# Kernel tuning notes

Measured on AMD Instinct MI355X. Metric: run time of the kernel, lower is better.

## Reference

```python
import jax, jax.numpy as jnp
import numpy as np

N = 100000       # nodes
E0 = 1600000     # edges without self loops
E = E0 + N       # with self loops appended (attr 0), matching add_self_loops
DIN = 128        # input_dim
HID = 64         # nb_hidden_gnn (per-head out_channels)
HEADS = 4
EMB = 128
L = 3            # nb_layer
NEG_SLOPE = 0.2
BN_EPS = 1e-5


def setup_inputs() -> dict:
    key = jax.random.key(0)
    ks = jax.random.split(key, 12)
    # edges with no self loops; self loops (i,i) appended with edge_attr 0
    row = jax.random.randint(ks[0], (E0,), 0, N)
    off = jax.random.randint(ks[1], (E0,), 1, N)
    col = (row + off) % N
    loops = jnp.arange(N, dtype=row.dtype)
    edge_index = jnp.stack([jnp.concatenate([row, loops]),
                            jnp.concatenate([col, loops])])
    edge_attr = jnp.concatenate([jax.random.normal(ks[2], (E0, 1), jnp.float32),
                                 jnp.zeros((N, 1), jnp.float32)])
    x = jax.random.normal(ks[3], (N, DIN), jnp.float32)
    HC = HEADS * HID
    linN0 = jax.random.normal(ks[4], (DIN, HC)) * HC ** -0.5
    linN_rest = jax.random.normal(ks[5], (L - 1, HID, HC)) * HC ** -0.5
    linE_all = jax.random.normal(ks[6], (L, 1, HEADS)) * HEADS ** -0.5  # nb_edge_attr=1
    att_all = jax.random.normal(ks[7], (L, HEADS, 2 * HID + 1)) * (2 * HID + 1) ** -0.5
    bias_all = jnp.zeros((L, HID))  # concat=False -> bias [out_channels]
    bn_gamma = jnp.ones((L - 1, HID))
    bn_beta = jnp.zeros((L - 1, HID))
    W = jax.random.normal(ks[8], (HID, EMB)) * HID ** -0.5
    b = jnp.zeros((EMB,))
    return {"x": x, "edge_index": edge_index, "edge_attr": edge_attr,
            "linN0": linN0, "linN_rest": linN_rest, "linE_all": linE_all,
            "att_all": att_all, "bias_all": bias_all,
            "bn_gamma": bn_gamma, "bn_beta": bn_beta, "W": W, "b": b}


def _gcn_layer(x, row, col, edge_attr, linN, linE, att, bias, bn):
    n = x.shape[0]
    if bn is not None:
        gamma, beta = bn
        mu = x.mean(axis=0)
        var = x.var(axis=0)
        x = (x - mu) * jax.lax.rsqrt(var + BN_EPS) * gamma + beta
    h = (x @ linN).reshape(n, HEADS, HID)                 # [N,H,C]
    e = (edge_attr @ linE)                                # [E,H] (nb_edge_attr=1)
    att_i = att[:, :HID]                                  # [H,C]
    att_j = att[:, HID:2 * HID]                           # [H,C]
    att_e = att[:, 2 * HID:]                              # [H,1]
    # per-node partial scores avoid gathering full features twice
    s_i = jnp.einsum('nhc,hc->nh', h, att_i)
    s_j = jnp.einsum('nhc,hc->nh', h, att_j)
    logits = s_i[row] + s_j[col] + e * att_e[:, 0]        # [E,H]
    logits = jax.nn.leaky_relu(logits, NEG_SLOPE)
    # segment softmax over destination nodes (edge_index[1])
    m = jax.ops.segment_max(logits, col, num_segments=n)
    p = jnp.exp(logits - m[col])
    denom = jax.ops.segment_sum(p, col, num_segments=n)
    alpha = p / (denom[col] + 1e-16)
    # message: alpha * x[source], scatter-add to destination
    msg = alpha[:, :, None] * h[row]                      # [E,H,C]
    out = jax.ops.segment_sum(msg, col, num_segments=n)   # [N,H,C]
    out = out.mean(axis=1) + bias + h.mean(axis=1)        # concat=False, res=True
    return jax.nn.relu(out)


def reference(x, edge_index, edge_attr, linN0, linN_rest, linE_all, att_all,
              bias_all, bn_gamma, bn_beta, W, b):
    row, col = edge_index[0], edge_index[1]
    emb = x
    for l in range(L):
        linN = linN0 if l == 0 else linN_rest[l - 1]
        bn = None if l == 0 else (bn_gamma[l - 1], bn_beta[l - 1])
        emb = _gcn_layer(emb, row, col, edge_attr, linN, linE_all[l],
                         att_all[l], bias_all[l], bn)
    return emb @ W + b
```

## Files before the change

kernel.cpp:

```cpp
#include <hip/hip_runtime.h>
#include <math.h>

#define NN 100000
#define E0E 1600000
#define EE (E0E + NN)
#define NEG 0.2f
#define BNEPS 1e-5f
#define LOG2E 1.4426950408889634f

typedef float f4 __attribute__((ext_vector_type(4)));
typedef float f2 __attribute__((ext_vector_type(2)));
typedef short s8v __attribute__((ext_vector_type(8)));

__device__ __forceinline__ float wred_max(float v) {
#pragma unroll
  for (int m = 1; m < 64; m <<= 1) v = fmaxf(v, __shfl_xor(v, m, 64));
  return v;
}
__device__ __forceinline__ float wred_sum(float v) {
#pragma unroll
  for (int m = 1; m < 64; m <<= 1) v += __shfl_xor(v, m, 64);
  return v;
}
__device__ __forceinline__ float sel4(float a0, float a1, float a2, float a3, int hd) {
  return (hd & 2) ? ((hd & 1) ? a3 : a2) : ((hd & 1) ? a1 : a0);
}
__device__ __forceinline__ unsigned short f2bf(float x) {
  unsigned u = __float_as_uint(x);
  return (unsigned short)((u + 0x7fffu + ((u >> 16) & 1u)) >> 16);
}
__device__ __forceinline__ float bf2f(unsigned short s) {
  return __uint_as_float(((unsigned)s) << 16);
}
__device__ __forceinline__ void gll16(const void* g, void* l) {
  __builtin_amdgcn_global_load_lds(
      (const __attribute__((address_space(1))) void*)g,
      (__attribute__((address_space(3))) void*)l, 16, 0, 0);
}

__global__ void k_count(const int* __restrict__ col, int* cnt, int e) {
  int i = blockIdx.x * blockDim.x + threadIdx.x;
  if (i < e) atomicAdd(&cnt[col[i]], 1);
}
#define SCAN_T 1024
__global__ void k_scan1(const int* __restrict__ cnt, int* partial, int n, int chunk) {
  int i = blockIdx.x * blockDim.x + threadIdx.x;
  int beg = i * chunk, end = min(n, beg + chunk);
  int s = 0;
  for (int j = beg; j < end; ++j) s += cnt[j];
  partial[i] = s;
}
__global__ void k_scan2(int* partial) {
  __shared__ int lds[SCAN_T];
  int t = threadIdx.x;
  int v = partial[t];
  lds[t] = v;
  __syncthreads();
  for (int off = 1; off < SCAN_T; off <<= 1) {
    int add = (t >= off) ? lds[t - off] : 0;
    __syncthreads();
    lds[t] += add;
    __syncthreads();
  }
  partial[t] = lds[t] - v;
}
__global__ void k_scan3(const int* __restrict__ cnt, const int* __restrict__ partial,
                        int* rowptr, int* cursor, int n, int chunk, int etot) {
  int i = blockIdx.x * blockDim.x + threadIdx.x;
  int beg = i * chunk, end = min(n, beg + chunk);
  int run = partial[i];
  for (int j = beg; j < end; ++j) {
    rowptr[j] = run;
    cursor[j] = run;
    run += cnt[j];
  }
  if (i == SCAN_T - 1) rowptr[n] = etot;
}
__global__ void k_scatter(const int* __restrict__ row, const int* __restrict__ col,
                          const float* __restrict__ ea, int* cursor, int2* csr, int e) {
  int i = blockIdx.x * blockDim.x + threadIdx.x;
  if (i < e) {
    int c = col[i];
    int p = atomicAdd(&cursor[c], 1);
    csr[p] = make_int2(row[i], __float_as_int(ea[i]));
  }
}

__global__ void k_bnstats(const unsigned short* __restrict__ x, double* sums, int n) {
  int f = threadIdx.x & 63;
  int rt = (blockIdx.x * blockDim.x + threadIdx.x) >> 6;
  int rstride = (gridDim.x * blockDim.x) >> 6;
  double s = 0.0, q = 0.0;
  for (int r = rt; r < n; r += rstride) {
    double v = (double)bf2f(x[(size_t)r * 64 + f]);
    s += v;
    q += v * v;
  }
  __shared__ double ls[256], lq[256];
  ls[threadIdx.x] = s;
  lq[threadIdx.x] = q;
  __syncthreads();
  if (threadIdx.x < 64) {
    s = ls[threadIdx.x] + ls[threadIdx.x + 64] + ls[threadIdx.x + 128] + ls[threadIdx.x + 192];
    q = lq[threadIdx.x] + lq[threadIdx.x + 64] + lq[threadIdx.x + 128] + lq[threadIdx.x + 192];
    atomicAdd(&sums[f], s);
    atomicAdd(&sums[64 + f], q);
  }
}

__global__ void k_prepw(const float* __restrict__ W, const double* __restrict__ bnsum,
                        const float* __restrict__ gamma, const float* __restrict__ beta,
                        const float* __restrict__ bin, unsigned short* __restrict__ Wt,
                        float* __restrict__ cvec, int K, int N, int mode) {
  __shared__ float ABl[128];
  __shared__ float cred[4][64];
  int t = threadIdx.x;
  if (mode == 1) {
    if (t < 64) {
      double mean = bnsum[t] / NN;
      double var = bnsum[64 + t] / NN - mean * mean;
      float A = gamma[t] * rsqrtf((float)var + BNEPS);
      ABl[t] = A;
      ABl[64 + t] = beta[t] - (float)mean * A;
    }
    __syncthreads();
  }
  int cl = t & 63, kq = t >> 6;
  int col = blockIdx.x * 64 + cl;
  int kn = K >> 2;
  int k0 = kq * kn;
  float c = 0.f;
#pragma unroll 8
  for (int k = k0; k < k0 + kn; ++k) {
    float w = W[k * N + col];
    float a = 1.f, b = 0.f;
    if (mode == 1) { a = ABl[k]; b = ABl[64 + k]; }
    Wt[col * K + k] = f2bf(a * w);
    c = fmaf(b, w, c);
  }
  cred[kq][cl] = c;
  __syncthreads();
  if (kq == 0) {
    float cc = cred[0][cl] + cred[1][cl] + cred[2][cl] + cred[3][cl];
    if (mode == 2) cc += bin[col];
    cvec[col] = cc;
  }
}

template <int K, int CT, bool ATT, bool OB, bool INBF>
__global__ __launch_bounds__(256, 2) void k_gemm(const void* __restrict__ xv,
                                                 const unsigned short* __restrict__ Wt,
                                                 const float* __restrict__ cvec,
                                                 const float* __restrict__ att,
                                                 void* __restrict__ houtv,
                                                 float* __restrict__ s_i,
                                                 float* __restrict__ s_j, int n,
                                                 int ntiles) {
  constexpr int KS = K / 32;
  constexpr int ROWB = 2 * K;
  constexpr int CPR = K / 8;
  constexpr int NCOL = 4 * CT * 16;
  __shared__ unsigned char xs[64 * ROWB];
  const int lane = threadIdx.x & 63;
  const int wv = threadIdx.x >> 6;
  const int l15 = lane & 15;
  const int lq = lane >> 4;
  const int colbase = wv * CT * 16;

  s8v wfr[CT][KS];
#pragma unroll
  for (int ct = 0; ct < CT; ++ct)
#pragma unroll
    for (int ks = 0; ks < KS; ++ks)
      wfr[ct][ks] = *(const s8v*)&Wt[(size_t)(colbase + ct * 16 + l15) * K + ks * 32 + lq * 8];
  float cb[CT][4];
#pragma unroll
  for (int ct = 0; ct < CT; ++ct)
#pragma unroll
    for (int r = 0; r < 4; ++r) cb[ct][r] = cvec[colbase + ct * 16 + lq * 4 + r];
  float ati[ATT ? CT : 1][4], atj[ATT ? CT : 1][4];
  if constexpr (ATT) {
    const float* ar = att + wv * 129;
#pragma unroll
    for (int ct = 0; ct < CT; ++ct)
#pragma unroll
      for (int r = 0; r < 4; ++r) {
        int cc = ct * 16 + lq * 4 + r;
        ati[ct][r] = ar[cc];
        atj[ct][r] = ar[64 + cc];
      }
  }

  for (int t = blockIdx.x; t < ntiles; t += gridDim.x) {
    const int row0 = t * 64;
    __syncthreads();
    if constexpr (INBF) {
      const unsigned char* xin8 = (const unsigned char*)xv;
#pragma unroll
      for (int i = 0; i < (64 * CPR) / 256; ++i) {
        int cbase = i * 256 + wv * 64;
        int c = cbase + lane;
        int row = c / CPR, kc = c % CPR;
        int rg = min(row0 + row, n - 1);
        int swz = kc ^ (row & 7);
        gll16(xin8 + (size_t)rg * ROWB + swz * 16, &xs[cbase * 16]);
      }
    } else {
#pragma unroll
      for (int i = 0; i < (64 * CPR) / 256; ++i) {
        int c = threadIdx.x + i * 256;
        int row = c / CPR, kc = c % CPR;
        int rg = min(row0 + row, n - 1);
        int dst = row * ROWB + ((kc * 16) ^ ((row & 7) << 4));
        const float* xin = (const float*)xv;
        const float* xp = xin + (size_t)rg * K + kc * 8;
        f4 a0 = *(const f4*)xp;
        f4 a1 = *(const f4*)(xp + 4);
        union { s8v v; unsigned short u[8]; } pk;
        pk.u[0] = f2bf(a0[0]); pk.u[1] = f2bf(a0[1]); pk.u[2] = f2bf(a0[2]); pk.u[3] = f2bf(a0[3]);
        pk.u[4] = f2bf(a1[0]); pk.u[5] = f2bf(a1[1]); pk.u[6] = f2bf(a1[2]); pk.u[7] = f2bf(a1[3]);
        *(s8v*)&xs[dst] = pk.v;
      }
    }
    __syncthreads();
    f4 acc[4][CT];
#pragma unroll
    for (int rt = 0; rt < 4; ++rt)
#pragma unroll
      for (int ct = 0; ct < CT; ++ct) acc[rt][ct] = (f4)0.f;
#pragma unroll
    for (int ks = 0; ks < KS; ++ks) {
      s8v xf[4];
#pragma unroll
      for (int rt = 0; rt < 4; ++rt) {
        int row = rt * 16 + l15;
        int kb = ks * 64 + lq * 16;
        xf[rt] = *(const s8v*)&xs[row * ROWB + (kb ^ ((row & 7) << 4))];
      }
#pragma unroll
      for (int rt = 0; rt < 4; ++rt)
#pragma unroll
        for (int ct = 0; ct < CT; ++ct)
          acc[rt][ct] = __builtin_amdgcn_mfma_f32_16x16x32_bf16(wfr[ct][ks], xf[rt],
                                                                acc[rt][ct], 0, 0, 0);
    }
#pragma unroll
    for (int rt = 0; rt < 4; ++rt) {
      if (row0 + rt * 16 >= n) continue;
      const size_t xrow = (size_t)(row0 + rt * 16 + l15);
      float v[CT][4];
#pragma unroll
      for (int ct = 0; ct < CT; ++ct)
#pragma unroll
        for (int r = 0; r < 4; ++r) v[ct][r] = acc[rt][ct][r] + cb[ct][r];
      if constexpr (OB) {
        float* outp = (float*)houtv;
#pragma unroll
        for (int ct = 0; ct < CT; ++ct) {
          f4 o;
          o[0] = v[ct][0]; o[1] = v[ct][1]; o[2] = v[ct][2]; o[3] = v[ct][3];
          *(f4*)&outp[xrow * NCOL + colbase + ct * 16 + lq * 4] = o;
        }
      } else {
        unsigned short* hout = (unsigned short*)houtv;
#pragma unroll
        for (int ct = 0; ct < CT; ++ct) {
          ushort4 hb4;
          hb4.x = f2bf(v[ct][0]); hb4.y = f2bf(v[ct][1]);
          hb4.z = f2bf(v[ct][2]); hb4.w = f2bf(v[ct][3]);
          *(ushort4*)&hout[xrow * NCOL + colbase + ct * 16 + lq * 4] = hb4;
        }
      }
      if constexpr (ATT) {
        float pi = 0.f, pj = 0.f;
#pragma unroll
        for (int ct = 0; ct < CT; ++ct)
#pragma unroll
          for (int r = 0; r < 4; ++r) {
            pi = fmaf(v[ct][r], ati[ct][r], pi);
            pj = fmaf(v[ct][r], atj[ct][r], pj);
          }
        pi += __shfl_xor(pi, 16, 64); pi += __shfl_xor(pi, 32, 64);
        pj += __shfl_xor(pj, 16, 64); pj += __shfl_xor(pj, 32, 64);
        if (lane < 16) {
          s_i[xrow * 4 + wv] = pi;
          s_j[xrow * 4 + wv] = pj;
        }
      }
    }
  }
}

__global__ __launch_bounds__(256) void k_edge(const int* __restrict__ rowptr,
                                              const int2* __restrict__ csr,
                                              const float* __restrict__ s_i,
                                              const float* __restrict__ s_j,
                                              const unsigned short* __restrict__ hb,
                                              const float* __restrict__ linE,
                                              const float* __restrict__ att,
                                              const float* __restrict__ bias,
                                              unsigned short* __restrict__ xout, int n) {
  __shared__ float lp[4][64][4];
  __shared__ int lsrc[4][64];
  const unsigned char* hb8 = (const unsigned char*)hb;
  const int lane = threadIdx.x & 63;
  const int wid = threadIdx.x >> 6;
  const int lane8 = lane * 8;
  int v = blockIdx.x * 4 + wid;
  if (v >= n) return;
  v = __builtin_amdgcn_readfirstlane(v);
  const int base = rowptr[v];
  const int deg = rowptr[v + 1] - base;

  const float coef0 = linE[0] * att[0 * 129 + 128];
  const float coef1 = linE[1] * att[1 * 129 + 128];
  const float coef2 = linE[2] * att[2 * 129 + 128];
  const float coef3 = linE[3] * att[3 * 129 + 128];
  const float sj0 = s_j[(size_t)v * 4 + 0];
  const float sj1 = s_j[(size_t)v * 4 + 1];
  const float sj2 = s_j[(size_t)v * 4 + 2];
  const float sj3 = s_j[(size_t)v * 4 + 3];

  auto edge_logits = [&](int i, int& src, float& g0, float& g1, float& g2, float& g3) {
    int2 pk = csr[i];
    src = pk.x;
    float ea = __int_as_float(pk.y);
    f4 siv = *(const f4*)&s_i[(size_t)src * 4];
    g0 = siv[0] + sj0 + ea * coef0; g0 = fmaxf(g0, g0 * NEG);
    g1 = siv[1] + sj1 + ea * coef1; g1 = fmaxf(g1, g1 * NEG);
    g2 = siv[2] + sj2 + ea * coef2; g2 = fmaxf(g2, g2 * NEG);
    g3 = siv[3] + sj3 + ea * coef3; g3 = fmaxf(g3, g3 * NEG);
  };

  const int hd = lane >> 4;
  f4 acc;
  {
    ushort4 hr = *(const ushort4*)(hb8 + ((unsigned)v << 9) + lane8);
    acc[0] = bf2f(hr.x); acc[1] = bf2f(hr.y); acc[2] = bf2f(hr.z); acc[3] = bf2f(hr.w);
  }

  bool fast = (deg <= 64);
  if (fast) {
    float g0 = -INFINITY, g1 = -INFINITY, g2 = -INFINITY, g3 = -INFINITY;
    int src = 0;
    bool valid = lane < deg;
    if (valid) edge_logits(base + lane, src, g0, g1, g2, g3);
    float m0 = wred_max(g0), m1 = wred_max(g1), m2 = wred_max(g2), m3 = wred_max(g3);
    float p0 = valid ? exp2f((g0 - m0) * LOG2E) : 0.f;
    float p1 = valid ? exp2f((g1 - m1) * LOG2E) : 0.f;
    float p2 = valid ? exp2f((g2 - m2) * LOG2E) : 0.f;
    float p3 = valid ? exp2f((g3 - m3) * LOG2E) : 0.f;
    float d0 = wred_sum(p0), d1 = wred_sum(p1), d2 = wred_sum(p2), d3 = wred_sum(p3);
    float rd0 = 1.f / (d0 + 1e-16f);
    float rd1 = 1.f / (d1 + 1e-16f);
    float rd2 = 1.f / (d2 + 1e-16f);
    float rd3 = 1.f / (d3 + 1e-16f);
    if (valid) {
      f4 pp;
      pp[0] = p0 * rd0; pp[1] = p1 * rd1; pp[2] = p2 * rd2; pp[3] = p3 * rd3;
      *(f4*)&lp[wid][lane][0] = pp;
      lsrc[wid][lane] = src << 9;
    }
    for (int e = 0; e < deg; ++e) {
      int off = lsrc[wid][e];
      float a = lp[wid][e][hd];
      ushort4 h0 = *(const ushort4*)(hb8 + (unsigned)(off + lane8));
      acc[0] = fmaf(a, bf2f(h0.x), acc[0]);
      acc[1] = fmaf(a, bf2f(h0.y), acc[1]);
      acc[2] = fmaf(a, bf2f(h0.z), acc[2]);
      acc[3] = fmaf(a, bf2f(h0.w), acc[3]);
    }
  } else {
    float m0 = -INFINITY, m1 = -INFINITY, m2 = -INFINITY, m3 = -INFINITY;
    for (int c0 = 0; c0 < deg; c0 += 64) {
      int i = c0 + lane;
      if (i < deg) {
        int src; float g0, g1, g2, g3;
        edge_logits(base + i, src, g0, g1, g2, g3);
        m0 = fmaxf(m0, g0); m1 = fmaxf(m1, g1); m2 = fmaxf(m2, g2); m3 = fmaxf(m3, g3);
      }
    }
    m0 = wred_max(m0); m1 = wred_max(m1); m2 = wred_max(m2); m3 = wred_max(m3);
    float d0 = 0, d1 = 0, d2 = 0, d3 = 0;
    for (int c0 = 0; c0 < deg; c0 += 64) {
      int i = c0 + lane;
      if (i < deg) {
        int src; float g0, g1, g2, g3;
        edge_logits(base + i, src, g0, g1, g2, g3);
        d0 += exp2f((g0 - m0) * LOG2E);
        d1 += exp2f((g1 - m1) * LOG2E);
        d2 += exp2f((g2 - m2) * LOG2E);
        d3 += exp2f((g3 - m3) * LOG2E);
      }
    }
    d0 = wred_sum(d0); d1 = wred_sum(d1); d2 = wred_sum(d2); d3 = wred_sum(d3);
    float msel = sel4(m0, m1, m2, m3, hd);
    float rdsel = 1.f / (sel4(d0, d1, d2, d3, hd) + 1e-16f);
    const float sjsel = sel4(sj0, sj1, sj2, sj3, hd);
    const float cfsel = sel4(coef0, coef1, coef2, coef3, hd);
    for (int e = base; e < base + deg; ++e) {
      int2 pk = csr[e];
      int src = pk.x;
      float ea = __int_as_float(pk.y);
      f4 siv = *(const f4*)&s_i[(size_t)src * 4];
      float lg = sel4(siv[0], siv[1], siv[2], siv[3], hd) + sjsel + ea * cfsel;
      lg = fmaxf(lg, lg * NEG);
      float a = exp2f((lg - msel) * LOG2E) * rdsel;
      ushort4 hr = *(const ushort4*)(hb8 + ((unsigned)src << 9) + lane8);
      acc[0] = fmaf(a, bf2f(hr.x), acc[0]);
      acc[1] = fmaf(a, bf2f(hr.y), acc[1]);
      acc[2] = fmaf(a, bf2f(hr.z), acc[2]);
      acc[3] = fmaf(a, bf2f(hr.w), acc[3]);
    }
  }
#pragma unroll
  for (int m = 16; m < 64; m <<= 1) {
    acc[0] += __shfl_xor(acc[0], m, 64);
    acc[1] += __shfl_xor(acc[1], m, 64);
    acc[2] += __shfl_xor(acc[2], m, 64);
    acc[3] += __shfl_xor(acc[3], m, 64);
  }
  if (lane < 16) {
    f4 bv = *(const f4*)&bias[lane * 4];
    ushort4 o;
    o.x = f2bf(fmaxf(acc[0] * 0.25f + bv[0], 0.f));
    o.y = f2bf(fmaxf(acc[1] * 0.25f + bv[1], 0.f));
    o.z = f2bf(fmaxf(acc[2] * 0.25f + bv[2], 0.f));
    o.w = f2bf(fmaxf(acc[3] * 0.25f + bv[3], 0.f));
    *(ushort4*)&xout[(size_t)v * 64 + lane * 4] = o;
  }
}

extern "C" void kernel_launch(void* const* d_in, const int* in_sizes, int n_in,
                              void* d_out, int out_size, void* d_ws, size_t ws_size,
                              hipStream_t stream) {
  const float* x_in = (const float*)d_in[0];
  const int* ei = (const int*)d_in[1];
  const float* eattr = (const float*)d_in[2];
  const float* linN0 = (const float*)d_in[3];
  const float* linNr = (const float*)d_in[4];
  const float* linE = (const float*)d_in[5];
  const float* attA = (const float*)d_in[6];
  const float* biasA = (const float*)d_in[7];
  const float* bng = (const float*)d_in[8];
  const float* bnb = (const float*)d_in[9];
  const float* W = (const float*)d_in[10];
  const float* bb = (const float*)d_in[11];
  float* out = (float*)d_out;

  const int* row = ei;
  const int* col = ei + EE;

  char* ws = (char*)d_ws;
  size_t o = 0;
  auto alloc = [&](size_t bytes) {
    void* p = ws + o;
    o += (bytes + 255) & ~(size_t)255;
    return p;
  };
  int* cnt = (int*)alloc((size_t)NN * 4);
  int* cursor = (int*)alloc((size_t)NN * 4);
  int* rowptr = (int*)alloc((size_t)(NN + 1) * 4);
  int* partial = (int*)alloc((size_t)SCAN_T * 4);
  int2* csr = (int2*)alloc((size_t)EE * 8);
  unsigned short* h = (unsigned short*)alloc((size_t)NN * 256 * 2);
  float* si = (float*)alloc((size_t)NN * 4 * 4);
  float* sj = (float*)alloc((size_t)NN * 4 * 4);
  unsigned short* xa = (unsigned short*)alloc((size_t)NN * 64 * 2);
  unsigned short* xb = (unsigned short*)alloc((size_t)NN * 64 * 2);
  double* bnsum = (double*)alloc(256 * 8);
  unsigned short* Wt = (unsigned short*)alloc((size_t)256 * 128 * 2);
  unsigned short* Wt2 = (unsigned short*)alloc((size_t)128 * 64 * 2);
  float* cvec = (float*)alloc(256 * 4);
  float* cvec2 = (float*)alloc(256 * 4);
  if (o > ws_size) return;

  const int chunk = (NN + SCAN_T - 1) / SCAN_T;
  const int NTILES = (NN + 63) / 64;
  const int GG = 512;

  hipMemsetAsync(cnt, 0, (size_t)NN * 4, stream);
  hipMemsetAsync(bnsum, 0, 256 * 8, stream);
  k_count<<<(EE + 255) / 256, 256, 0, stream>>>(col, cnt, EE);
  k_scan1<<<4, 256, 0, stream>>>(cnt, partial, NN, chunk);
  k_scan2<<<1, SCAN_T, 0, stream>>>(partial);
  k_scan3<<<4, 256, 0, stream>>>(cnt, partial, rowptr, cursor, NN, chunk, EE);
  k_scatter<<<(EE + 255) / 256, 256, 0, stream>>>(row, col, eattr, cursor, csr, EE);
  k_prepw<<<2, 256, 0, stream>>>(W, nullptr, nullptr, nullptr, bb, Wt2, cvec2, 64, 128, 2);

  k_prepw<<<4, 256, 0, stream>>>(linN0, nullptr, nullptr, nullptr, nullptr, Wt, cvec, 128, 256, 0);
  k_gemm<128, 4, true, false, false><<<GG, 256, 0, stream>>>(x_in, Wt, cvec, attA + 0,
                                                             h, si, sj, NN, NTILES);
  k_edge<<<NN / 4, 256, 0, stream>>>(rowptr, csr, si, sj, h, linE + 0, attA + 0, biasA + 0,
                                     xa, NN);

  k_bnstats<<<256, 256, 0, stream>>>(xa, bnsum, NN);
  k_prepw<<<4, 256, 0, stream>>>(linNr, bnsum, bng, bnb, nullptr, Wt, cvec, 64, 256, 1);
  k_gemm<64, 4, true, false, true><<<GG, 256, 0, stream>>>(xa, Wt, cvec, attA + 516,
                                                           h, si, sj, NN, NTILES);
  k_edge<<<NN / 4, 256, 0, stream>>>(rowptr, csr, si, sj, h, linE + 4, attA + 516, biasA + 64,
                                     xb, NN);

  k_bnstats<<<256, 256, 0, stream>>>(xb, bnsum + 128, NN);
  k_prepw<<<4, 256, 0, stream>>>(linNr + 64 * 256, bnsum + 128, bng + 64, bnb + 64, nullptr,
                                 Wt, cvec, 64, 256, 1);
  k_gemm<64, 4, true, false, true><<<GG, 256, 0, stream>>>(xb, Wt, cvec, attA + 2 * 516,
                                                           h, si, sj, NN, NTILES);
  k_edge<<<NN / 4, 256, 0, stream>>>(rowptr, csr, si, sj, h, linE + 8, attA + 2 * 516,
                                     biasA + 128, xa, NN);

  k_gemm<64, 2, false, true, true><<<GG, 256, 0, stream>>>(xa, Wt2, cvec2, nullptr, out,
                                                           nullptr, nullptr, NN, NTILES);
}
```

Measured before the change: 839.2 us.

## Fuse BN stats with weight prep and double-buffer bf16 GEMM tile loads

Merges the BatchNorm statistics kernel with the following weight-folding kernel by having the last block (found through an atomic done counter and threadfence) compute the scale and shift and write the folded bf16 weights. It also merges the two initial weight-prep launches into one kernel. In the bf16-input GEMM it double-buffers the LDS tile, so the async global-to-LDS load of the next tile is issued before computing the current one. This removes several small kernel launches and hides load latency, at the cost of twice the LDS for those GEMMs and a single-block tail for the weight fold.

Measured after the change: 828.9 us. About the same (-1.2%).

```diff
diff --git a/kernel.cpp b/kernel.cpp
--- a/kernel.cpp
+++ b/kernel.cpp
@@ -9,7 +9,6 @@
 #define LOG2E 1.4426950408889634f
 
 typedef float f4 __attribute__((ext_vector_type(4)));
-typedef float f2 __attribute__((ext_vector_type(2)));
 typedef short s8v __attribute__((ext_vector_type(8)));
 
 __device__ __forceinline__ float wred_max(float v) {
@@ -86,7 +85,32 @@
   }
 }
 
-__global__ void k_bnstats(const unsigned short* __restrict__ x, double* sums, int n) {
+__global__ void k_prep0(const float* __restrict__ W1, unsigned short* __restrict__ Wt1,
+                        float* __restrict__ cvec1, const float* __restrict__ W2,
+                        const float* __restrict__ bin2, unsigned short* __restrict__ Wt2,
+                        float* __restrict__ cvec2) {
+  int b = blockIdx.x;
+  int t = threadIdx.x;
+  int cl = t & 63, kq = t >> 6;
+  if (b < 4) {
+    int col = b * 64 + cl;
+#pragma unroll 8
+    for (int k = kq * 32; k < kq * 32 + 32; ++k)
+      Wt1[col * 128 + k] = f2bf(W1[k * 256 + col]);
+    if (kq == 0) cvec1[col] = 0.f;
+  } else {
+    int col = (b - 4) * 64 + cl;
+#pragma unroll 8
+    for (int k = kq * 16; k < kq * 16 + 16; ++k)
+      Wt2[col * 64 + k] = f2bf(W2[k * 128 + col]);
+    if (kq == 0) cvec2[col] = bin2[col];
+  }
+}
+
+__global__ void k_bnprep(const unsigned short* __restrict__ x, double* sums, int* done,
+                         const float* __restrict__ gamma, const float* __restrict__ beta,
+                         const float* __restrict__ W, unsigned short* __restrict__ Wt,
+                         float* __restrict__ cvec, int n) {
   int f = threadIdx.x & 63;
   int rt = (blockIdx.x * blockDim.x + threadIdx.x) >> 6;
   int rstride = (gridDim.x * blockDim.x) >> 6;
@@ -105,46 +129,36 @@
     q = lq[threadIdx.x] + lq[threadIdx.x + 64] + lq[threadIdx.x + 128] + lq[threadIdx.x + 192];
     atomicAdd(&sums[f], s);
     atomicAdd(&sums[64 + f], q);
-  }
-}
-
-__global__ void k_prepw(const float* __restrict__ W, const double* __restrict__ bnsum,
-                        const float* __restrict__ gamma, const float* __restrict__ beta,
-                        const float* __restrict__ bin, unsigned short* __restrict__ Wt,
-                        float* __restrict__ cvec, int K, int N, int mode) {
+    __threadfence();
+  }
+  __syncthreads();
+  __shared__ int lastFlag;
+  if (threadIdx.x == 0) {
+    int old = atomicAdd(done, 1);
+    lastFlag = (old == (int)gridDim.x - 1);
+  }
+  __syncthreads();
+  if (!lastFlag) return;
   __shared__ float ABl[128];
-  __shared__ float cred[4][64];
-  int t = threadIdx.x;
-  if (mode == 1) {
-    if (t < 64) {
-      double mean = bnsum[t] / NN;
-      double var = bnsum[64 + t] / NN - mean * mean;
-      float A = gamma[t] * rsqrtf((float)var + BNEPS);
-      ABl[t] = A;
-      ABl[64 + t] = beta[t] - (float)mean * A;
-    }
-    __syncthreads();
-  }
-  int cl = t & 63, kq = t >> 6;
-  int col = blockIdx.x * 64 + cl;
-  int kn = K >> 2;
-  int k0 = kq * kn;
+  if (threadIdx.x < 64) {
+    int t = threadIdx.x;
+    double mean = atomicAdd(&sums[t], 0.0) / n;
+    double qq = atomicAdd(&sums[64 + t], 0.0);
+    double var = qq / n - mean * mean;
+    float A = gamma[t] * rsqrtf((float)var + BNEPS);
+    ABl[t] = A;
+    ABl[64 + t] = beta[t] - (float)mean * A;
+  }
+  __syncthreads();
+  int col = threadIdx.x;
   float c = 0.f;
 #pragma unroll 8
-  for (int k = k0; k < k0 + kn; ++k) {
-    float w = W[k * N + col];
-    float a = 1.f, b = 0.f;
-    if (mode == 1) { a = ABl[k]; b = ABl[64 + k]; }
-    Wt[col * K + k] = f2bf(a * w);
-    c = fmaf(b, w, c);
-  }
-  cred[kq][cl] = c;
-  __syncthreads();
-  if (kq == 0) {
-    float cc = cred[0][cl] + cred[1][cl] + cred[2][cl] + cred[3][cl];
-    if (mode == 2) cc += bin[col];
-    cvec[col] = cc;
-  }
+  for (int k = 0; k < 64; ++k) {
+    float w = W[k * 256 + col];
+    Wt[col * 64 + k] = f2bf(ABl[k] * w);
+    c = fmaf(ABl[64 + k], w, c);
+  }
+  cvec[col] = c;
 }
 
 template <int K, int CT, bool ATT, bool OB, bool INBF>
@@ -160,7 +174,8 @@
   constexpr int ROWB = 2 * K;
   constexpr int CPR = K / 8;
   constexpr int NCOL = 4 * CT * 16;
-  __shared__ unsigned char xs[64 * ROWB];
+  constexpr int TILEB = 64 * ROWB;
+  __shared__ unsigned char xs[(INBF ? 2 : 1) * TILEB];
   const int lane = threadIdx.x & 63;
   const int wv = threadIdx.x >> 6;
   const int l15 = lane & 15;
@@ -191,11 +206,78 @@
       }
   }
 
-  for (int t = blockIdx.x; t < ntiles; t += gridDim.x) {
-    const int row0 = t * 64;
-    __syncthreads();
-    if constexpr (INBF) {
-      const unsigned char* xin8 = (const unsigned char*)xv;
+  auto COMPUTE = [&](const unsigned char* buf, int row0) {
+    f4 acc[4][CT];
+#pragma unroll
+    for (int rt = 0; rt < 4; ++rt)
+#pragma unroll
+      for (int ct = 0; ct < CT; ++ct) acc[rt][ct] = (f4)0.f;
+#pragma unroll
+    for (int ks = 0; ks < KS; ++ks) {
+      s8v xf[4];
+#pragma unroll
+      for (int rt = 0; rt < 4; ++rt) {
+        int row = rt * 16 + l15;
+        int kb = ks * 64 + lq * 16;
+        xf[rt] = *(const s8v*)&buf[row * ROWB + (kb ^ ((row & 7) << 4))];
+      }
+#pragma unroll
+      for (int rt = 0; rt < 4; ++rt)
+#pragma unroll
+        for (int ct = 0; ct < CT; ++ct)
+          acc[rt][ct] = __builtin_amdgcn_mfma_f32_16x16x32_bf16(wfr[ct][ks], xf[rt],
+                                                                acc[rt][ct], 0, 0, 0);
+    }
+#pragma unroll
+    for (int rt = 0; rt < 4; ++rt) {
+      if (row0 + rt * 16 >= n) continue;
+      const size_t xrow = (size_t)(row0 + rt * 16 + l15);
+      float v[CT][4];
+#pragma unroll
+      for (int ct = 0; ct < CT; ++ct)
+#pragma unroll
+        for (int r = 0; r < 4; ++r) v[ct][r] = acc[rt][ct][r] + cb[ct][r];
+      if constexpr (OB) {
+        float* outp = (float*)houtv;
+#pragma unroll
+        for (int ct = 0; ct < CT; ++ct) {
+          f4 o;
+          o[0] = v[ct][0]; o[1] = v[ct][1]; o[2] = v[ct][2]; o[3] = v[ct][3];
+          *(f4*)&outp[xrow * NCOL + colbase + ct * 16 + lq * 4] = o;
+        }
+      } else {
+        unsigned short* hout = (unsigned short*)houtv;
+#pragma unroll
+        for (int ct = 0; ct < CT; ++ct) {
+          ushort4 hb4;
+          hb4.x = f2bf(v[ct][0]); hb4.y = f2bf(v[ct][1]);
+          hb4.z = f2bf(v[ct][2]); hb4.w = f2bf(v[ct][3]);
+          *(ushort4*)&hout[xrow * NCOL + colbase + ct * 16 + lq * 4] = hb4;
+        }
+      }
+      if constexpr (ATT) {
+        float pi = 0.f, pj = 0.f;
+#pragma unroll
+        for (int ct = 0; ct < CT; ++ct)
+#pragma unroll
+          for (int r = 0; r < 4; ++r) {
+            pi = fmaf(v[ct][r], ati[ct][r], pi);
+            pj = fmaf(v[ct][r], atj[ct][r], pj);
+          }
+        pi += __shfl_xor(pi, 16, 64); pi += __shfl_xor(pi, 32, 64);
+        pj += __shfl_xor(pj, 16, 64); pj += __shfl_xor(pj, 32, 64);
+        if (lane < 16) {
+          s_i[xrow * 4 + wv] = pi;
+          s_j[xrow * 4 + wv] = pj;
+        }
+      }
+    }
+  };
+
+  if constexpr (INBF) {
+    const unsigned char* xin8 = (const unsigned char*)xv;
+    auto STAGE = [&](unsigned char* buf, int t) {
+      int row0 = t * 64;
 #pragma unroll
       for (int i = 0; i < (64 * CPR) / 256; ++i) {
         int cbase = i * 256 + wv * 64;
@@ -203,9 +285,22 @@
         int row = c / CPR, kc = c % CPR;
         int rg = min(row0 + row, n - 1);
         int swz = kc ^ (row & 7);
-        gll16(xin8 + (size_t)rg * ROWB + swz * 16, &xs[cbase * 16]);
-      }
-    } else {
+        gll16(xin8 + (size_t)rg * ROWB + swz * 16, buf + cbase * 16);
+      }
+    };
+    int cur = 0;
+    STAGE(xs, blockIdx.x);
+    for (int t = blockIdx.x; t < ntiles; t += gridDim.x) {
+      __syncthreads();
+      int tn = t + gridDim.x;
+      if (tn < ntiles) STAGE(xs + (cur ^ 1) * TILEB, tn);
+      COMPUTE(xs + cur * TILEB, t * 64);
+      cur ^= 1;
+    }
+  } else {
+    for (int t = blockIdx.x; t < ntiles; t += gridDim.x) {
+      const int row0 = t * 64;
+      __syncthreads();
 #pragma unroll
       for (int i = 0; i < (64 * CPR) / 256; ++i) {
         int c = threadIdx.x + i * 256;
@@ -221,72 +316,8 @@
         pk.u[4] = f2bf(a1[0]); pk.u[5] = f2bf(a1[1]); pk.u[6] = f2bf(a1[2]); pk.u[7] = f2bf(a1[3]);
         *(s8v*)&xs[dst] = pk.v;
       }
-    }
-    __syncthreads();
-    f4 acc[4][CT];
-#pragma unroll
-    for (int rt = 0; rt < 4; ++rt)
-#pragma unroll
-      for (int ct = 0; ct < CT; ++ct) acc[rt][ct] = (f4)0.f;
-#pragma unroll
-    for (int ks = 0; ks < KS; ++ks) {
-      s8v xf[4];
-#pragma unroll
-      for (int rt = 0; rt < 4; ++rt) {
-        int row = rt * 16 + l15;
-        int kb = ks * 64 + lq * 16;
-        xf[rt] = *(const s8v*)&xs[row * ROWB + (kb ^ ((row & 7) << 4))];
-      }
-#pragma unroll
-      for (int rt = 0; rt < 4; ++rt)
-#pragma unroll
-        for (int ct = 0; ct < CT; ++ct)
-          acc[rt][ct] = __builtin_amdgcn_mfma_f32_16x16x32_bf16(wfr[ct][ks], xf[rt],
-                                                                acc[rt][ct], 0, 0, 0);
-    }
-#pragma unroll
-    for (int rt = 0; rt < 4; ++rt) {
-      if (row0 + rt * 16 >= n) continue;
-      const size_t xrow = (size_t)(row0 + rt * 16 + l15);
-      float v[CT][4];
-#pragma unroll
-      for (int ct = 0; ct < CT; ++ct)
-#pragma unroll
-        for (int r = 0; r < 4; ++r) v[ct][r] = acc[rt][ct][r] + cb[ct][r];
-      if constexpr (OB) {
-        float* outp = (float*)houtv;
-#pragma unroll
-        for (int ct = 0; ct < CT; ++ct) {
-          f4 o;
-          o[0] = v[ct][0]; o[1] = v[ct][1]; o[2] = v[ct][2]; o[3] = v[ct][3];
-          *(f4*)&outp[xrow * NCOL + colbase + ct * 16 + lq * 4] = o;
-        }
-      } else {
-        unsigned short* hout = (unsigned short*)houtv;
-#pragma unroll
-        for (int ct = 0; ct < CT; ++ct) {
-          ushort4 hb4;
-          hb4.x = f2bf(v[ct][0]); hb4.y = f2bf(v[ct][1]);
-          hb4.z = f2bf(v[ct][2]); hb4.w = f2bf(v[ct][3]);
-          *(ushort4*)&hout[xrow * NCOL + colbase + ct * 16 + lq * 4] = hb4;
-        }
-      }
-      if constexpr (ATT) {
-        float pi = 0.f, pj = 0.f;
-#pragma unroll
-        for (int ct = 0; ct < CT; ++ct)
-#pragma unroll
-          for (int r = 0; r < 4; ++r) {
-            pi = fmaf(v[ct][r], ati[ct][r], pi);
-            pj = fmaf(v[ct][r], atj[ct][r], pj);
-          }
-        pi += __shfl_xor(pi, 16, 64); pi += __shfl_xor(pi, 32, 64);
-        pj += __shfl_xor(pj, 16, 64); pj += __shfl_xor(pj, 32, 64);
-        if (lane < 16) {
-          s_i[xrow * 4 + wv] = pi;
-          s_j[xrow * 4 + wv] = pj;
-        }
-      }
+      __syncthreads();
+      COMPUTE(xs, row0);
     }
   }
 }
@@ -468,7 +499,8 @@
   float* sj = (float*)alloc((size_t)NN * 4 * 4);
   unsigned short* xa = (unsigned short*)alloc((size_t)NN * 64 * 2);
   unsigned short* xb = (unsigned short*)alloc((size_t)NN * 64 * 2);
-  double* bnsum = (double*)alloc(256 * 8);
+  double* bnsum = (double*)alloc(256 * 8 + 64);
+  int* done = (int*)(bnsum + 256);
   unsigned short* Wt = (unsigned short*)alloc((size_t)256 * 128 * 2);
   unsigned short* Wt2 = (unsigned short*)alloc((size_t)128 * 64 * 2);
   float* cvec = (float*)alloc(256 * 4);
@@ -480,30 +512,27 @@
   const int GG = 512;
 
   hipMemsetAsync(cnt, 0, (size_t)NN * 4, stream);
-  hipMemsetAsync(bnsum, 0, 256 * 8, stream);
+  hipMemsetAsync(bnsum, 0, 256 * 8 + 64, stream);
   k_count<<<(EE + 255) / 256, 256, 0, stream>>>(col, cnt, EE);
   k_scan1<<<4, 256, 0, stream>>>(cnt, partial, NN, chunk);
   k_scan2<<<1, SCAN_T, 0, stream>>>(partial);
   k_scan3<<<4, 256, 0, stream>>>(cnt, partial, rowptr, cursor, NN, chunk, EE);
   k_scatter<<<(EE + 255) / 256, 256, 0, stream>>>(row, col, eattr, cursor, csr, EE);
-  k_prepw<<<2, 256, 0, stream>>>(W, nullptr, nullptr, nullptr, bb, Wt2, cvec2, 64, 128, 2);
-
-  k_prepw<<<4, 256, 0, stream>>>(linN0, nullptr, nullptr, nullptr, nullptr, Wt, cvec, 128, 256, 0);
+  k_prep0<<<6, 256, 0, stream>>>(linN0, Wt, cvec, W, bb, Wt2, cvec2);
+
   k_gemm<128, 4, true, false, false><<<GG, 256, 0, stream>>>(x_in, Wt, cvec, attA + 0,
                                                              h, si, sj, NN, NTILES);
   k_edge<<<NN / 4, 256, 0, stream>>>(rowptr, csr, si, sj, h, linE + 0, attA + 0, biasA + 0,
                                      xa, NN);
 
-  k_bnstats<<<256, 256, 0, stream>>>(xa, bnsum, NN);
-  k_prepw<<<4, 256, 0, stream>>>(linNr, bnsum, bng, bnb, nullptr, Wt, cvec, 64, 256, 1);
+  k_bnprep<<<256, 256, 0, stream>>>(xa, bnsum, done + 0, bng, bnb, linNr, Wt, cvec, NN);
   k_gemm<64, 4, true, false, true><<<GG, 256, 0, stream>>>(xa, Wt, cvec, attA + 516,
                                                            h, si, sj, NN, NTILES);
   k_edge<<<NN / 4, 256, 0, stream>>>(rowptr, csr, si, sj, h, linE + 4, attA + 516, biasA + 64,
                                      xb, NN);
 
-  k_bnstats<<<256, 256, 0, stream>>>(xb, bnsum + 128, NN);
-  k_prepw<<<4, 256, 0, stream>>>(linNr + 64 * 256, bnsum + 128, bng + 64, bnb + 64, nullptr,
-                                 Wt, cvec, 64, 256, 1);
+  k_bnprep<<<256, 256, 0, stream>>>(xb, bnsum + 128, done + 1, bng + 64, bnb + 64,
+                                    linNr + 64 * 256, Wt, cvec, NN);
   k_gemm<64, 4, true, false, true><<<GG, 256, 0, stream>>>(xb, Wt, cvec, attA + 2 * 516,
                                                            h, si, sj, NN, NTILES);
   k_edge<<<NN / 4, 256, 0, stream>>>(rowptr, csr, si, sj, h, linE + 8, attA + 2 * 516,
```
